# Kernel optimization log

Measured on AMD Instinct MI355X. Metric: run time of the kernel, lower is better.

## Reference

```python
import jax, jax.numpy as jnp
import numpy as np

N_NODES = 50000
EPS = 1e-5


def sage_conv_max(x, src, dst, W_l, b_l, W_r):
    # PyG SAGEConv(aggr='max'): out = lin_l(max_j x_j) + lin_r(x_i)
    msg = x[src]                                   # [E, d] gather
    agg = jnp.full((x.shape[0], x.shape[1]), -jnp.inf, dtype=x.dtype)
    agg = agg.at[dst].max(msg)                     # scatter-max over edges
    agg = jnp.where(jnp.isneginf(agg), 0.0, agg)   # isolated nodes -> 0 (PyG convention)
    return agg @ W_l.T + b_l + x @ W_r.T


def batch_norm(x, gamma, beta):
    mean = jnp.mean(x, axis=0)
    var = jnp.var(x, axis=0)
    return (x - mean) * jax.lax.rsqrt(var + EPS) * gamma + beta


def setup_inputs() -> dict:
    key = jax.random.key(0)
    ks = jax.random.split(key, 10)
    d_in, d_h, d_out = 128, 128, 32
    s = lambda fan: 1.0 / np.sqrt(fan)
    return {
        "x": jax.random.normal(ks[0], (N_NODES, d_in), dtype=jnp.float32),
        "edge_index": jax.random.randint(ks[1], (2, 800000), 0, N_NODES, dtype=jnp.int32),
        "W_l1": jax.random.uniform(ks[2], (d_h, d_in), jnp.float32, -s(d_in), s(d_in)),
        "b_l1": jnp.zeros((d_h,), jnp.float32),
        "W_r1": jax.random.uniform(ks[3], (d_h, d_in), jnp.float32, -s(d_in), s(d_in)),
        "gamma1": jnp.ones((d_h,), jnp.float32),
        "beta1": jnp.zeros((d_h,), jnp.float32),
        "W_l2": jax.random.uniform(ks[4], (d_out, d_h), jnp.float32, -s(d_h), s(d_h)),
        "b_l2": jnp.zeros((d_out,), jnp.float32),
        "W_r2": jax.random.uniform(ks[5], (d_out, d_h), jnp.float32, -s(d_h), s(d_h)),
    }


def reference(x, edge_index, W_l1, b_l1, W_r1, gamma1, beta1, W_l2, b_l2, W_r2):
    src, dst = edge_index[0], edge_index[1]
    h = sage_conv_max(x, src, dst, W_l1, b_l1, W_r1)
    h = batch_norm(h, gamma1, beta1)
    h = jax.nn.relu(h)
    # dropout is identity at inference
    return sage_conv_max(h, src, dst, W_l2, b_l2, W_r2)
```

## Files before the change

### kernel.cpp

```cpp
#include <hip/hip_runtime.h>
#include <math.h>
#include <float.h>

#define N_NODES 50000
#define N_EDGES 800000
#define DH 128
#define NB 196
#define EB 4096
#define NBUCK 98
#define BSH 9
#define CAP 80
#define SEGC 9216
#define CELLS_PER_BUCKET (NB * CAP)

typedef __attribute__((ext_vector_type(8))) short bf16x8;
typedef __attribute__((ext_vector_type(4))) float f32x4;

static __device__ __forceinline__ unsigned short f2bf(float f) {
  unsigned int u = __float_as_uint(f);
  u = (u + 0x7fff + ((u >> 16) & 1)) >> 16;
  return (unsigned short)u;
}

__global__ __launch_bounds__(256) void setup_kernel(
    const int* __restrict__ src, const int* __restrict__ dst,
    unsigned int* __restrict__ pairs,
    const float* __restrict__ x, const float* __restrict__ Wl1,
    const float* __restrict__ Wr1, const float* __restrict__ Wl2,
    const float* __restrict__ Wr2, unsigned int* __restrict__ x_bf,
    unsigned short* __restrict__ Wcat1, unsigned short* __restrict__ Wcat2,
    float* __restrict__ gsums) {
  const int b = blockIdx.x, tid = threadIdx.x;
  if (b < NB) {
    __shared__ int cur[NBUCK];
    if (tid < NBUCK) cur[tid] = 0;
    __syncthreads();
#pragma unroll
    for (int it = 0; it < EB / 256; ++it) {
      int e = b * EB + it * 256 + tid;
      if (e < N_EDGES) {
        int d = dst[e];
        int bk = d >> BSH;
        int p = atomicAdd(&cur[bk], 1);
        if (p < CAP)
          pairs[(size_t)(bk * NB + b) * CAP + p] =
              (unsigned)src[e] | ((unsigned)(d & 511) << 16);
      }
    }
    __syncthreads();
    for (int s = tid; s < NBUCK * CAP; s += 256) {
      int bk = s / CAP, slot = s - bk * CAP;
      if (slot >= cur[bk])
        pairs[(size_t)(bk * NB + b) * CAP + slot] = 0x80000000u;
    }
  } else if (b < NB + 6250) {
    int i = (b - NB) * 256 + tid;
    float4 v = ((const float4*)x)[i];
    uint2 o;
    o.x = (unsigned int)f2bf(v.x) | ((unsigned int)f2bf(v.y) << 16);
    o.y = (unsigned int)f2bf(v.z) | ((unsigned int)f2bf(v.w) << 16);
    ((uint2*)x_bf)[i] = o;
  } else if (b < NB + 6410) {
    int i = (b - NB - 6250) * 256 + tid;
    if (i < 32768) {
      int n = i >> 8, k = i & 255;
      float w = (k < 128) ? Wl1[n * 128 + k] : Wr1[n * 128 + (k - 128)];
      Wcat1[i] = f2bf(w);
    } else if (i < 40960) {
      int j = i - 32768;
      int n = j >> 8, k = j & 255;
      float w = (k < 128) ? Wl2[n * 128 + k] : Wr2[n * 128 + (k - 128)];
      Wcat2[j] = f2bf(w);
    }
  } else {
#pragma unroll
    for (int i = 0; i < 8; ++i) gsums[i * 256 + tid] = 0.f;
  }
}

__global__ __launch_bounds__(1024) void bucket_sort(const unsigned int* __restrict__ pairs,
                                                    unsigned int* __restrict__ rowinfo,
                                                    int* __restrict__ elist) {
  __shared__ int hist[512], sc[512], cpos[512];
  const int b = blockIdx.x, tid = threadIdx.x;
  const size_t s0 = (size_t)b * CELLS_PER_BUCKET;
  if (tid < 512) hist[tid] = 0;
  __syncthreads();
  for (int p = tid; p < CELLS_PER_BUCKET; p += 1024) {
    unsigned int pr = pairs[s0 + p];
    if ((int)pr >= 0) atomicAdd(&hist[(pr >> 16) & 511], 1);
  }
  __syncthreads();
  if (tid < 512) sc[tid] = hist[tid];
  __syncthreads();
  for (int off = 1; off < 512; off <<= 1) {
    int x = (tid < 512 && tid >= off) ? sc[tid - off] : 0;
    __syncthreads();
    if (tid < 512) sc[tid] += x;
    __syncthreads();
  }
  if (tid < 512) {
    int excl = sc[tid] - hist[tid];
    cpos[tid] = excl;
    int node = (b << BSH) + tid;
    if (node < N_NODES)
      rowinfo[node] = (unsigned)(b * SEGC + excl) | ((unsigned)hist[tid] << 20);
  }
  __syncthreads();
  for (int p = tid; p < CELLS_PER_BUCKET; p += 1024) {
    unsigned int pr = pairs[s0 + p];
    if ((int)pr >= 0) {
      int loc = atomicAdd(&cpos[(pr >> 16) & 511], 1);
      elist[b * SEGC + loc] = (int)(pr & 0xffffu);
    }
  }
}

template <bool BN>
__global__ __launch_bounds__(256) void agg_max_bf16(const uint4* __restrict__ feat4,
                                                    const unsigned int* __restrict__ rowinfo,
                                                    const int* __restrict__ elist,
                                                    const float* __restrict__ gsums,
                                                    const float* __restrict__ gamma,
                                                    const float* __restrict__ beta,
                                                    uint4* __restrict__ out4) {
  __shared__ float s_scale[128], s_shift[128];
  if (BN) {
    int t = threadIdx.x;
    if (t < 128) {
      float sm = 0.f, sq = 0.f;
#pragma unroll
      for (int r = 0; r < 8; ++r) {
        sm += gsums[r * 256 + t];
        sq += gsums[r * 256 + 128 + t];
      }
      const float inv = 1.f / (float)N_NODES;
      float mean = sm * inv;
      float var = sq * inv - mean * mean;
      float sc = gamma[t] * rsqrtf(var + 1e-5f);
      s_scale[t] = sc;
      s_shift[t] = beta[t] - mean * sc;
    }
    __syncthreads();
  }

  int node = blockIdx.x * 4 + (threadIdx.x >> 6);
  int lane = threadIdx.x & 63;
  int eslot = lane >> 4;
  int fq = lane & 15;
  unsigned int info = rowinfo[node];
  int e0 = (int)(info & 0xFFFFFu);
  int deg = (int)(info >> 20);
  int e1 = e0 + deg;
  float m[8];
#pragma unroll
  for (int j = 0; j < 8; ++j) m[j] = -FLT_MAX;

  if (deg > 0) {
    const int last = e1 - 1;
    for (int base = e0; base < e1; base += 16) {
      int idx[4];
#pragma unroll
      for (int q = 0; q < 4; ++q) {
        int e = base + q * 4 + eslot;
        if (e > last) e = last;
        idx[q] = elist[e];
      }
      uint4 v[4];
#pragma unroll
      for (int q = 0; q < 4; ++q) v[q] = feat4[(size_t)idx[q] * 16 + fq];
#pragma unroll
      for (int q = 0; q < 4; ++q) {
        const unsigned int* pv = (const unsigned int*)&v[q];
#pragma unroll
        for (int c = 0; c < 4; ++c) {
          m[2 * c]     = fmaxf(m[2 * c],     __uint_as_float(pv[c] << 16));
          m[2 * c + 1] = fmaxf(m[2 * c + 1], __uint_as_float(pv[c] & 0xffff0000u));
        }
      }
    }
  }

#pragma unroll
  for (int j = 0; j < 8; ++j) {
    m[j] = fmaxf(m[j], __shfl_xor(m[j], 16, 64));
    m[j] = fmaxf(m[j], __shfl_xor(m[j], 32, 64));
  }
  if (eslot == 0) {
    if (deg == 0) {
#pragma unroll
      for (int j = 0; j < 8; ++j) m[j] = 0.f;
    } else if (BN) {
#pragma unroll
      for (int j = 0; j < 8; ++j) {
        int col = fq * 8 + j;
        m[j] = fmaxf(m[j] * s_scale[col] + s_shift[col], 0.f);
      }
    }
    uint4 o;
    o.x = (unsigned)f2bf(m[0]) | ((unsigned)f2bf(m[1]) << 16);
    o.y = (unsigned)f2bf(m[2]) | ((unsigned)f2bf(m[3]) << 16);
    o.z = (unsigned)f2bf(m[4]) | ((unsigned)f2bf(m[5]) << 16);
    o.w = (unsigned)f2bf(m[6]) | ((unsigned)f2bf(m[7]) << 16);
    out4[(size_t)node * 16 + fq] = o;
  }
}

#define ASTR 264

template <int NT, bool BF16OUT, bool STATS, bool BNIN>
__global__ __launch_bounds__(256) void gemm_mfma(
    const unsigned short* __restrict__ Aa, const unsigned short* __restrict__ Ab,
    const unsigned short* __restrict__ Wcat, const float* __restrict__ bias,
    unsigned short* __restrict__ outb, float* __restrict__ outf,
    float* __restrict__ gsums, const float* __restrict__ gamma,
    const float* __restrict__ beta, int N) {
  __shared__ unsigned short Alds[128 * ASTR];
  __shared__ float s_sum[128], s_sq[128];
  __shared__ float s_scale[128], s_shift[128];
  const int tid = threadIdx.x;
  const int rowBase = blockIdx.x * 128;

  if (STATS && tid < 128) { s_sum[tid] = 0.f; s_sq[tid] = 0.f; }
  if (BNIN) {
    if (tid < 128) {
      float sm = 0.f, sq = 0.f;
#pragma unroll
      for (int r = 0; r < 8; ++r) {
        sm += gsums[r * 256 + tid];
        sq += gsums[r * 256 + 128 + tid];
      }
      const float inv = 1.f / (float)N_NODES;
      float mean = sm * inv;
      float var = sq * inv - mean * mean;
      float sc = gamma[tid] * rsqrtf(var + 1e-5f);
      s_scale[tid] = sc;
      s_shift[tid] = beta[tid] - mean * sc;
    }
    __syncthreads();
  }

#pragma unroll
  for (int it = 0; it < 16; ++it) {
    int f = tid + it * 256;
    int r = f >> 5;
    int seg = f & 31;
    int n = rowBase + r;
    if (n >= N) n = N - 1;
    const unsigned short* src = (seg < 16)
        ? (Aa + (size_t)n * 128 + seg * 8)
        : (Ab + (size_t)n * 128 + (seg - 16) * 8);
    int4 d = *(const int4*)src;
    if (BNIN && seg >= 16) {
      int kb = (seg - 16) * 8;
      unsigned int* dp = (unsigned int*)&d;
#pragma unroll
      for (int c = 0; c < 4; ++c) {
        int k0 = kb + 2 * c;
        float lo = __uint_as_float(dp[c] << 16);
        float hi = __uint_as_float(dp[c] & 0xffff0000u);
        lo = fmaxf(lo * s_scale[k0] + s_shift[k0], 0.f);
        hi = fmaxf(hi * s_scale[k0 + 1] + s_shift[k0 + 1], 0.f);
        dp[c] = (unsigned)f2bf(lo) | ((unsigned)f2bf(hi) << 16);
      }
    }
    *(int4*)(&Alds[r * ASTR + seg * 8]) = d;
  }
  __syncthreads();

  const int wv = tid >> 6;
  const int lane = tid & 63;
  const int ln15 = lane & 15;
  const int quad = lane >> 4;
  const int m0 = wv * 32;

  f32x4 acc[2][NT] = {};

#pragma unroll
  for (int ks = 0; ks < 8; ++ks) {
    const int k0 = ks * 32;
    bf16x8 a0 = *(const bf16x8*)(&Alds[(m0 + ln15) * ASTR + k0 + quad * 8]);
    bf16x8 a1 = *(const bf16x8*)(&Alds[(m0 + 16 + ln15) * ASTR + k0 + quad * 8]);
#pragma unroll
    for (int nt = 0; nt < NT; ++nt) {
      bf16x8 b = *(const bf16x8*)(Wcat + (size_t)(nt * 16 + ln15) * 256 + k0 + quad * 8);
      acc[0][nt] = __builtin_amdgcn_mfma_f32_16x16x32_bf16(a0, b, acc[0][nt], 0, 0, 0);
      acc[1][nt] = __builtin_amdgcn_mfma_f32_16x16x32_bf16(a1, b, acc[1][nt], 0, 0, 0);
    }
  }

  const int ldo = NT * 16;
#pragma unroll
  for (int nt = 0; nt < NT; ++nt) {
    int col = nt * 16 + ln15;
    float bv = bias[col];
    float psum = 0.f, psq = 0.f;
#pragma unroll
    for (int mt = 0; mt < 2; ++mt) {
#pragma unroll
      for (int i = 0; i < 4; ++i) {
        int r = rowBase + m0 + mt * 16 + quad * 4 + i;
        if (r < N) {
          float val = acc[mt][nt][i] + bv;
          if (STATS) { psum += val; psq += val * val; }
          if (BF16OUT)
            outb[(size_t)r * ldo + col] = f2bf(val);
          else
            outf[(size_t)r * ldo + col] = val;
        }
      }
    }
    if (STATS) {
      atomicAdd(&s_sum[col], psum);
      atomicAdd(&s_sq[col], psq);
    }
  }
  if (STATS) {
    __syncthreads();
    if (tid < 128) {
      int rep = blockIdx.x & 7;
      atomicAdd(&gsums[rep * 256 + tid], s_sum[tid]);
      atomicAdd(&gsums[rep * 256 + 128 + tid], s_sq[tid]);
    }
  }
}

extern "C" void kernel_launch(void* const* d_in, const int* in_sizes, int n_in,
                              void* d_out, int out_size, void* d_ws, size_t ws_size,
                              hipStream_t stream) {
  (void)in_sizes; (void)n_in; (void)out_size; (void)ws_size;
  const float* x     = (const float*)d_in[0];
  const int*   eidx  = (const int*)d_in[1];
  const float* W_l1  = (const float*)d_in[2];
  const float* b_l1  = (const float*)d_in[3];
  const float* W_r1  = (const float*)d_in[4];
  const float* gamma = (const float*)d_in[5];
  const float* beta  = (const float*)d_in[6];
  const float* W_l2  = (const float*)d_in[7];
  const float* b_l2  = (const float*)d_in[8];
  const float* W_r2  = (const float*)d_in[9];
  const int* srcp = eidx;
  const int* dstp = eidx + N_EDGES;
  float* out = (float*)d_out;

  int* wsi = (int*)d_ws;
  float* gsums   = (float*)wsi;
  unsigned int* rowinfo = (unsigned int*)(wsi + 2048);
  int*   elist   = wsi + 52064;
  unsigned int* pairs   = (unsigned int*)(wsi + 955232);
  unsigned int* x_bf    = (unsigned int*)(wsi + 2491872);
  unsigned int* agg_bf  = (unsigned int*)(wsi + 5691872);
  unsigned int* h_bf    = (unsigned int*)(wsi + 8891872);
  unsigned short* Wcat1 = (unsigned short*)(wsi + 12091872);
  unsigned short* Wcat2 = (unsigned short*)(wsi + 12108256);

  setup_kernel<<<dim3(NB + 6410 + 1), 256, 0, stream>>>(
      srcp, dstp, pairs, x, W_l1, W_r1, W_l2, W_r2, x_bf, Wcat1, Wcat2, gsums);

  bucket_sort<<<dim3(NBUCK), 1024, 0, stream>>>(pairs, rowinfo, elist);

  agg_max_bf16<false><<<dim3(N_NODES / 4), 256, 0, stream>>>(
      (const uint4*)x_bf, rowinfo, elist, nullptr, nullptr, nullptr, (uint4*)agg_bf);
  gemm_mfma<8, true, true, false><<<dim3(391), 256, 0, stream>>>(
      (const unsigned short*)agg_bf, (const unsigned short*)x_bf, Wcat1, b_l1,
      (unsigned short*)h_bf, nullptr, gsums, nullptr, nullptr, N_NODES);

  agg_max_bf16<true><<<dim3(N_NODES / 4), 256, 0, stream>>>(
      (const uint4*)h_bf, rowinfo, elist, gsums, gamma, beta, (uint4*)agg_bf);
  gemm_mfma<2, false, false, true><<<dim3(391), 256, 0, stream>>>(
      (const unsigned short*)agg_bf, (const unsigned short*)h_bf, Wcat2, b_l2,
      nullptr, out, gsums, gamma, beta, N_NODES);
}
```

Before: 222.4 us.

## Prefetch next edge batch in max aggregation; use wave-shuffle scan in bucket sort

The edge loop in the max-aggregation kernel now software-pipelines its gathers. It issues the feature loads for the next batch of 16 edges, plus the index loads for the batch after that, before reducing the current batch. This hides gather latency behind the max arithmetic, at the cost of extra registers for the second set of vectors. Separately, the 512-element prefix scan in bucket_sort is replaced by a warp-shuffle scan plus a small cross-wave scan. That removes about 18 block-wide barriers.

```diff
diff --git a/kernel.cpp b/kernel.cpp
--- a/kernel.cpp
+++ b/kernel.cpp
@@ -81,7 +81,8 @@
 __global__ __launch_bounds__(1024) void bucket_sort(const unsigned int* __restrict__ pairs,
                                                     unsigned int* __restrict__ rowinfo,
                                                     int* __restrict__ elist) {
-  __shared__ int hist[512], sc[512], cpos[512];
+  __shared__ int hist[512], cpos[512];
+  __shared__ int wsum[8];
   const int b = blockIdx.x, tid = threadIdx.x;
   const size_t s0 = (size_t)b * CELLS_PER_BUCKET;
   if (tid < 512) hist[tid] = 0;
@@ -91,20 +92,37 @@
     if ((int)pr >= 0) atomicAdd(&hist[(pr >> 16) & 511], 1);
   }
   __syncthreads();
-  if (tid < 512) sc[tid] = hist[tid];
-  __syncthreads();
-  for (int off = 1; off < 512; off <<= 1) {
-    int x = (tid < 512 && tid >= off) ? sc[tid - off] : 0;
-    __syncthreads();
-    if (tid < 512) sc[tid] += x;
-    __syncthreads();
-  }
+  int incl = 0, h = 0;
   if (tid < 512) {
-    int excl = sc[tid] - hist[tid];
+    const int l = tid & 63;
+    h = hist[tid];
+    incl = h;
+#pragma unroll
+    for (int off = 1; off < 64; off <<= 1) {
+      int t = __shfl_up(incl, off, 64);
+      if (l >= off) incl += t;
+    }
+    if (l == 63) wsum[tid >> 6] = incl;
+  }
+  __syncthreads();
+  if (tid < 64) {
+    int v = (tid < 8) ? wsum[tid] : 0;
+#pragma unroll
+    for (int off = 1; off < 8; off <<= 1) {
+      int t = __shfl_up(v, off, 64);
+      if (tid >= off) v += t;
+    }
+    if (tid < 8) wsum[tid] = v;
+  }
+  __syncthreads();
+  if (tid < 512) {
+    const int w = tid >> 6;
+    int tot = incl + ((w > 0) ? wsum[w - 1] : 0);
+    int excl = tot - h;
     cpos[tid] = excl;
     int node = (b << BSH) + tid;
     if (node < N_NODES)
-      rowinfo[node] = (unsigned)(b * SEGC + excl) | ((unsigned)hist[tid] << 20);
+      rowinfo[node] = (unsigned)(b * SEGC + excl) | ((unsigned)h << 20);
   }
   __syncthreads();
   for (int p = tid; p < CELLS_PER_BUCKET; p += 1024) {
@@ -158,25 +176,53 @@
 
   if (deg > 0) {
     const int last = e1 - 1;
-    for (int base = e0; base < e1; base += 16) {
-      int idx[4];
+    int idxN[4];
+#pragma unroll
+    for (int q = 0; q < 4; ++q) {
+      int e = e0 + q * 4 + eslot;
+      if (e > last) e = last;
+      idxN[q] = elist[e];
+    }
+    uint4 vC[4];
+#pragma unroll
+    for (int q = 0; q < 4; ++q)
+      vC[q] = feat4[(size_t)idxN[q] * 16 + fq];
+#pragma unroll
+    for (int q = 0; q < 4; ++q) {
+      int e = e0 + 16 + q * 4 + eslot;
+      if (e > last) e = last;
+      idxN[q] = elist[e];
+    }
+    for (int base = e0 + 16; base < e1; base += 16) {
+      uint4 vN[4];
+#pragma unroll
+      for (int q = 0; q < 4; ++q)
+        vN[q] = feat4[(size_t)idxN[q] * 16 + fq];
 #pragma unroll
       for (int q = 0; q < 4; ++q) {
-        int e = base + q * 4 + eslot;
+        int e = base + 16 + q * 4 + eslot;
         if (e > last) e = last;
-        idx[q] = elist[e];
-      }
-      uint4 v[4];
-#pragma unroll
-      for (int q = 0; q < 4; ++q) v[q] = feat4[(size_t)idx[q] * 16 + fq];
+        idxN[q] = elist[e];
+      }
 #pragma unroll
       for (int q = 0; q < 4; ++q) {
-        const unsigned int* pv = (const unsigned int*)&v[q];
+        const unsigned int* pv = (const unsigned int*)&vC[q];
 #pragma unroll
         for (int c = 0; c < 4; ++c) {
           m[2 * c]     = fmaxf(m[2 * c],     __uint_as_float(pv[c] << 16));
           m[2 * c + 1] = fmaxf(m[2 * c + 1], __uint_as_float(pv[c] & 0xffff0000u));
         }
+      }
+#pragma unroll
+      for (int q = 0; q < 4; ++q) vC[q] = vN[q];
+    }
+#pragma unroll
+    for (int q = 0; q < 4; ++q) {
+      const unsigned int* pv = (const unsigned int*)&vC[q];
+#pragma unroll
+      for (int c = 0; c < 4; ++c) {
+        m[2 * c]     = fmaxf(m[2 * c],     __uint_as_float(pv[c] << 16));
+        m[2 * c + 1] = fmaxf(m[2 * c + 1], __uint_as_float(pv[c] & 0xffff0000u));
       }
     }
   }
```

New measurement: 223.0 us. No clear change (+0.3%).

## Fuse max-aggregation into MFMA GEMM and use wave-shuffle scan in bucket sort

Applied to the files above, without the earlier changes.

The separate aggregation kernel is merged into the GEMM kernel. Each 64-row block gathers neighbour features, applies the max (and BN+ReLU for layer 2), and writes the aggregated row straight into LDS next to the self features, so the agg_bf buffer round-trip and two launches go away. The gather mapping changes from four edge slots per node with a cross-lane reduce to one 16-lane group per node walking edges serially. That gives fewer parallel loads in flight per node, and the tiles are half the size with more blocks. The bucket-sort prefix scan is also rewritten from an LDS Hillis-Steele scan with many barriers to a wave-shuffle scan.

```diff
diff --git a/kernel.cpp b/kernel.cpp
--- a/kernel.cpp
+++ b/kernel.cpp
@@ -12,6 +12,7 @@
 #define CAP 80
 #define SEGC 9216
 #define CELLS_PER_BUCKET (NB * CAP)
+#define NBLK 782
 
 typedef __attribute__((ext_vector_type(8))) short bf16x8;
 typedef __attribute__((ext_vector_type(4))) float f32x4;
@@ -81,7 +82,8 @@
 __global__ __launch_bounds__(1024) void bucket_sort(const unsigned int* __restrict__ pairs,
                                                     unsigned int* __restrict__ rowinfo,
                                                     int* __restrict__ elist) {
-  __shared__ int hist[512], sc[512], cpos[512];
+  __shared__ int hist[512], cpos[512];
+  __shared__ int wsum[8];
   const int b = blockIdx.x, tid = threadIdx.x;
   const size_t s0 = (size_t)b * CELLS_PER_BUCKET;
   if (tid < 512) hist[tid] = 0;
@@ -91,20 +93,37 @@
     if ((int)pr >= 0) atomicAdd(&hist[(pr >> 16) & 511], 1);
   }
   __syncthreads();
-  if (tid < 512) sc[tid] = hist[tid];
-  __syncthreads();
-  for (int off = 1; off < 512; off <<= 1) {
-    int x = (tid < 512 && tid >= off) ? sc[tid - off] : 0;
-    __syncthreads();
-    if (tid < 512) sc[tid] += x;
-    __syncthreads();
-  }
+  int incl = 0, h = 0;
   if (tid < 512) {
-    int excl = sc[tid] - hist[tid];
+    const int l = tid & 63;
+    h = hist[tid];
+    incl = h;
+#pragma unroll
+    for (int off = 1; off < 64; off <<= 1) {
+      int t = __shfl_up(incl, off, 64);
+      if (l >= off) incl += t;
+    }
+    if (l == 63) wsum[tid >> 6] = incl;
+  }
+  __syncthreads();
+  if (tid < 64) {
+    int v = (tid < 8) ? wsum[tid] : 0;
+#pragma unroll
+    for (int off = 1; off < 8; off <<= 1) {
+      int t = __shfl_up(v, off, 64);
+      if (tid >= off) v += t;
+    }
+    if (tid < 8) wsum[tid] = v;
+  }
+  __syncthreads();
+  if (tid < 512) {
+    const int w = tid >> 6;
+    int tot = incl + ((w > 0) ? wsum[w - 1] : 0);
+    int excl = tot - h;
     cpos[tid] = excl;
     int node = (b << BSH) + tid;
     if (node < N_NODES)
-      rowinfo[node] = (unsigned)(b * SEGC + excl) | ((unsigned)hist[tid] << 20);
+      rowinfo[node] = (unsigned)(b * SEGC + excl) | ((unsigned)h << 20);
   }
   __syncthreads();
   for (int p = tid; p < CELLS_PER_BUCKET; p += 1024) {
@@ -116,113 +135,26 @@
   }
 }
 
-template <bool BN>
-__global__ __launch_bounds__(256) void agg_max_bf16(const uint4* __restrict__ feat4,
-                                                    const unsigned int* __restrict__ rowinfo,
-                                                    const int* __restrict__ elist,
-                                                    const float* __restrict__ gsums,
-                                                    const float* __restrict__ gamma,
-                                                    const float* __restrict__ beta,
-                                                    uint4* __restrict__ out4) {
-  __shared__ float s_scale[128], s_shift[128];
-  if (BN) {
-    int t = threadIdx.x;
-    if (t < 128) {
-      float sm = 0.f, sq = 0.f;
-#pragma unroll
-      for (int r = 0; r < 8; ++r) {
-        sm += gsums[r * 256 + t];
-        sq += gsums[r * 256 + 128 + t];
-      }
-      const float inv = 1.f / (float)N_NODES;
-      float mean = sm * inv;
-      float var = sq * inv - mean * mean;
-      float sc = gamma[t] * rsqrtf(var + 1e-5f);
-      s_scale[t] = sc;
-      s_shift[t] = beta[t] - mean * sc;
-    }
-    __syncthreads();
-  }
-
-  int node = blockIdx.x * 4 + (threadIdx.x >> 6);
-  int lane = threadIdx.x & 63;
-  int eslot = lane >> 4;
-  int fq = lane & 15;
-  unsigned int info = rowinfo[node];
-  int e0 = (int)(info & 0xFFFFFu);
-  int deg = (int)(info >> 20);
-  int e1 = e0 + deg;
-  float m[8];
-#pragma unroll
-  for (int j = 0; j < 8; ++j) m[j] = -FLT_MAX;
-
-  if (deg > 0) {
-    const int last = e1 - 1;
-    for (int base = e0; base < e1; base += 16) {
-      int idx[4];
-#pragma unroll
-      for (int q = 0; q < 4; ++q) {
-        int e = base + q * 4 + eslot;
-        if (e > last) e = last;
-        idx[q] = elist[e];
-      }
-      uint4 v[4];
-#pragma unroll
-      for (int q = 0; q < 4; ++q) v[q] = feat4[(size_t)idx[q] * 16 + fq];
-#pragma unroll
-      for (int q = 0; q < 4; ++q) {
-        const unsigned int* pv = (const unsigned int*)&v[q];
-#pragma unroll
-        for (int c = 0; c < 4; ++c) {
-          m[2 * c]     = fmaxf(m[2 * c],     __uint_as_float(pv[c] << 16));
-          m[2 * c + 1] = fmaxf(m[2 * c + 1], __uint_as_float(pv[c] & 0xffff0000u));
-        }
-      }
-    }
-  }
-
-#pragma unroll
-  for (int j = 0; j < 8; ++j) {
-    m[j] = fmaxf(m[j], __shfl_xor(m[j], 16, 64));
-    m[j] = fmaxf(m[j], __shfl_xor(m[j], 32, 64));
-  }
-  if (eslot == 0) {
-    if (deg == 0) {
-#pragma unroll
-      for (int j = 0; j < 8; ++j) m[j] = 0.f;
-    } else if (BN) {
-#pragma unroll
-      for (int j = 0; j < 8; ++j) {
-        int col = fq * 8 + j;
-        m[j] = fmaxf(m[j] * s_scale[col] + s_shift[col], 0.f);
-      }
-    }
-    uint4 o;
-    o.x = (unsigned)f2bf(m[0]) | ((unsigned)f2bf(m[1]) << 16);
-    o.y = (unsigned)f2bf(m[2]) | ((unsigned)f2bf(m[3]) << 16);
-    o.z = (unsigned)f2bf(m[4]) | ((unsigned)f2bf(m[5]) << 16);
-    o.w = (unsigned)f2bf(m[6]) | ((unsigned)f2bf(m[7]) << 16);
-    out4[(size_t)node * 16 + fq] = o;
-  }
-}
-
 #define ASTR 264
 
-template <int NT, bool BF16OUT, bool STATS, bool BNIN>
-__global__ __launch_bounds__(256) void gemm_mfma(
-    const unsigned short* __restrict__ Aa, const unsigned short* __restrict__ Ab,
+template <int NT, bool BF16OUT, bool STATS, bool BN>
+__global__ __launch_bounds__(256) void fused_layer(
+    const uint4* __restrict__ feat4,
+    const unsigned short* __restrict__ Ab,
+    const unsigned int* __restrict__ rowinfo,
+    const int* __restrict__ elist,
     const unsigned short* __restrict__ Wcat, const float* __restrict__ bias,
     unsigned short* __restrict__ outb, float* __restrict__ outf,
     float* __restrict__ gsums, const float* __restrict__ gamma,
     const float* __restrict__ beta, int N) {
-  __shared__ unsigned short Alds[128 * ASTR];
+  __shared__ unsigned short Alds[64 * ASTR];
   __shared__ float s_sum[128], s_sq[128];
   __shared__ float s_scale[128], s_shift[128];
   const int tid = threadIdx.x;
-  const int rowBase = blockIdx.x * 128;
+  const int rowBase = blockIdx.x * 64;
 
   if (STATS && tid < 128) { s_sum[tid] = 0.f; s_sq[tid] = 0.f; }
-  if (BNIN) {
+  if (BN) {
     if (tid < 128) {
       float sm = 0.f, sq = 0.f;
 #pragma unroll
@@ -241,18 +173,14 @@
   }
 
 #pragma unroll
-  for (int it = 0; it < 16; ++it) {
+  for (int it = 0; it < 4; ++it) {
     int f = tid + it * 256;
-    int r = f >> 5;
-    int seg = f & 31;
+    int r = f >> 4, seg = f & 15;
     int n = rowBase + r;
     if (n >= N) n = N - 1;
-    const unsigned short* src = (seg < 16)
-        ? (Aa + (size_t)n * 128 + seg * 8)
-        : (Ab + (size_t)n * 128 + (seg - 16) * 8);
-    int4 d = *(const int4*)src;
-    if (BNIN && seg >= 16) {
-      int kb = (seg - 16) * 8;
+    int4 d = *(const int4*)(Ab + (size_t)n * 128 + seg * 8);
+    if (BN) {
+      int kb = seg * 8;
       unsigned int* dp = (unsigned int*)&d;
 #pragma unroll
       for (int c = 0; c < 4; ++c) {
@@ -264,28 +192,80 @@
         dp[c] = (unsigned)f2bf(lo) | ((unsigned)f2bf(hi) << 16);
       }
     }
-    *(int4*)(&Alds[r * ASTR + seg * 8]) = d;
-  }
-  __syncthreads();
+    *(int4*)(&Alds[r * ASTR + 128 + seg * 8]) = d;
+  }
 
   const int wv = tid >> 6;
+  const int g = (tid >> 4) & 3;
+  const int fq = tid & 15;
+#pragma unroll
+  for (int it = 0; it < 4; ++it) {
+    int r = it * 16 + wv * 4 + g;
+    int node = rowBase + r;
+    if (node >= N) node = N - 1;
+    unsigned int info = rowinfo[node];
+    int e0 = (int)(info & 0xFFFFFu);
+    int deg = (int)(info >> 20);
+    int e1 = e0 + deg;
+    const int last = e1 - 1;
+    float m[8];
+#pragma unroll
+    for (int j = 0; j < 8; ++j) m[j] = -FLT_MAX;
+    for (int base = e0; base < e1; base += 4) {
+      int idx[4];
+#pragma unroll
+      for (int q = 0; q < 4; ++q) {
+        int e = base + q;
+        if (e > last) e = last;
+        idx[q] = elist[e];
+      }
+      uint4 v[4];
+#pragma unroll
+      for (int q = 0; q < 4; ++q) v[q] = feat4[(size_t)idx[q] * 16 + fq];
+#pragma unroll
+      for (int q = 0; q < 4; ++q) {
+        const unsigned int* pv = (const unsigned int*)&v[q];
+#pragma unroll
+        for (int c = 0; c < 4; ++c) {
+          m[2 * c]     = fmaxf(m[2 * c],     __uint_as_float(pv[c] << 16));
+          m[2 * c + 1] = fmaxf(m[2 * c + 1], __uint_as_float(pv[c] & 0xffff0000u));
+        }
+      }
+    }
+    if (deg == 0) {
+#pragma unroll
+      for (int j = 0; j < 8; ++j) m[j] = 0.f;
+    } else if (BN) {
+#pragma unroll
+      for (int j = 0; j < 8; ++j) {
+        int col = fq * 8 + j;
+        m[j] = fmaxf(m[j] * s_scale[col] + s_shift[col], 0.f);
+      }
+    }
+    int4 o;
+    unsigned int* op = (unsigned int*)&o;
+    op[0] = (unsigned)f2bf(m[0]) | ((unsigned)f2bf(m[1]) << 16);
+    op[1] = (unsigned)f2bf(m[2]) | ((unsigned)f2bf(m[3]) << 16);
+    op[2] = (unsigned)f2bf(m[4]) | ((unsigned)f2bf(m[5]) << 16);
+    op[3] = (unsigned)f2bf(m[6]) | ((unsigned)f2bf(m[7]) << 16);
+    *(int4*)(&Alds[r * ASTR + fq * 8]) = o;
+  }
+  __syncthreads();
+
   const int lane = tid & 63;
   const int ln15 = lane & 15;
   const int quad = lane >> 4;
-  const int m0 = wv * 32;
-
-  f32x4 acc[2][NT] = {};
-
+  const int m0 = wv * 16;
+
+  f32x4 acc[NT] = {};
 #pragma unroll
   for (int ks = 0; ks < 8; ++ks) {
     const int k0 = ks * 32;
-    bf16x8 a0 = *(const bf16x8*)(&Alds[(m0 + ln15) * ASTR + k0 + quad * 8]);
-    bf16x8 a1 = *(const bf16x8*)(&Alds[(m0 + 16 + ln15) * ASTR + k0 + quad * 8]);
+    bf16x8 a = *(const bf16x8*)(&Alds[(m0 + ln15) * ASTR + k0 + quad * 8]);
 #pragma unroll
     for (int nt = 0; nt < NT; ++nt) {
       bf16x8 b = *(const bf16x8*)(Wcat + (size_t)(nt * 16 + ln15) * 256 + k0 + quad * 8);
-      acc[0][nt] = __builtin_amdgcn_mfma_f32_16x16x32_bf16(a0, b, acc[0][nt], 0, 0, 0);
-      acc[1][nt] = __builtin_amdgcn_mfma_f32_16x16x32_bf16(a1, b, acc[1][nt], 0, 0, 0);
+      acc[nt] = __builtin_amdgcn_mfma_f32_16x16x32_bf16(a, b, acc[nt], 0, 0, 0);
     }
   }
 
@@ -296,18 +276,15 @@
     float bv = bias[col];
     float psum = 0.f, psq = 0.f;
 #pragma unroll
-    for (int mt = 0; mt < 2; ++mt) {
-#pragma unroll
-      for (int i = 0; i < 4; ++i) {
-        int r = rowBase + m0 + mt * 16 + quad * 4 + i;
-        if (r < N) {
-          float val = acc[mt][nt][i] + bv;
-          if (STATS) { psum += val; psq += val * val; }
-          if (BF16OUT)
-            outb[(size_t)r * ldo + col] = f2bf(val);
-          else
-            outf[(size_t)r * ldo + col] = val;
-        }
+    for (int i = 0; i < 4; ++i) {
+      int r = rowBase + m0 + quad * 4 + i;
+      if (r < N) {
+        float val = acc[nt][i] + bv;
+        if (STATS) { psum += val; psq += val * val; }
+        if (BF16OUT)
+          outb[(size_t)r * ldo + col] = f2bf(val);
+        else
+          outf[(size_t)r * ldo + col] = val;
       }
     }
     if (STATS) {
@@ -349,7 +326,6 @@
   int*   elist   = wsi + 52064;
   unsigned int* pairs   = (unsigned int*)(wsi + 955232);
   unsigned int* x_bf    = (unsigned int*)(wsi + 2491872);
-  unsigned int* agg_bf  = (unsigned int*)(wsi + 5691872);
   unsigned int* h_bf    = (unsigned int*)(wsi + 8891872);
   unsigned short* Wcat1 = (unsigned short*)(wsi + 12091872);
   unsigned short* Wcat2 = (unsigned short*)(wsi + 12108256);
@@ -359,15 +335,11 @@
 
   bucket_sort<<<dim3(NBUCK), 1024, 0, stream>>>(pairs, rowinfo, elist);
 
-  agg_max_bf16<false><<<dim3(N_NODES / 4), 256, 0, stream>>>(
-      (const uint4*)x_bf, rowinfo, elist, nullptr, nullptr, nullptr, (uint4*)agg_bf);
-  gemm_mfma<8, true, true, false><<<dim3(391), 256, 0, stream>>>(
-      (const unsigned short*)agg_bf, (const unsigned short*)x_bf, Wcat1, b_l1,
+  fused_layer<8, true, true, false><<<dim3(NBLK), 256, 0, stream>>>(
+      (const uint4*)x_bf, (const unsigned short*)x_bf, rowinfo, elist, Wcat1, b_l1,
       (unsigned short*)h_bf, nullptr, gsums, nullptr, nullptr, N_NODES);
 
-  agg_max_bf16<true><<<dim3(N_NODES / 4), 256, 0, stream>>>(
-      (const uint4*)h_bf, rowinfo, elist, gsums, gamma, beta, (uint4*)agg_bf);
-  gemm_mfma<2, false, false, true><<<dim3(391), 256, 0, stream>>>(
-      (const unsigned short*)agg_bf, (const unsigned short*)h_bf, Wcat2, b_l2,
+  fused_layer<2, false, false, true><<<dim3(NBLK), 256, 0, stream>>>(
+      (const uint4*)h_bf, (const unsigned short*)h_bf, rowinfo, elist, Wcat2, b_l2,
       nullptr, out, gsums, gamma, beta, N_NODES);
 }
```

Measured after the change: 225.2 us. Within noise of the previous version (+1.3%).

## Split max-aggregation into feature slices with per-edge lanes; stage pair buckets in LDS

Applied to the files above, without the earlier changes.

The max-aggregation kernel now gives each block one 32-feature slice of 64 nodes. Sixteen lanes cover the slice and each 16-lane group walks one node's edges, four edges per step. Neighbouring block IDs share a slice, which is meant to improve L2 locality of the gathered feature columns, at the cost of narrower 4-byte loads instead of 16-byte loads. The setup kernel stages bucket pairs in LDS and writes each full cell once, replacing scattered global writes plus a separate padding pass. bucket_sort replaces its 512-element barrier-heavy scan with a wave-shuffle scan.

```diff
diff --git a/kernel.cpp b/kernel.cpp
--- a/kernel.cpp
+++ b/kernel.cpp
@@ -4,7 +4,6 @@
 
 #define N_NODES 50000
 #define N_EDGES 800000
-#define DH 128
 #define NB 196
 #define EB 4096
 #define NBUCK 98
@@ -12,6 +11,8 @@
 #define CAP 80
 #define SEGC 9216
 #define CELLS_PER_BUCKET (NB * CAP)
+#define GCHUNKS 784
+#define GGRID (GCHUNKS * 4)
 
 typedef __attribute__((ext_vector_type(8))) short bf16x8;
 typedef __attribute__((ext_vector_type(4))) float f32x4;
@@ -32,7 +33,9 @@
     float* __restrict__ gsums) {
   const int b = blockIdx.x, tid = threadIdx.x;
   if (b < NB) {
+    __shared__ unsigned int lp[NBUCK * CAP];
     __shared__ int cur[NBUCK];
+    for (int s = tid; s < NBUCK * CAP; s += 256) lp[s] = 0x80000000u;
     if (tid < NBUCK) cur[tid] = 0;
     __syncthreads();
 #pragma unroll
@@ -43,15 +46,13 @@
         int bk = d >> BSH;
         int p = atomicAdd(&cur[bk], 1);
         if (p < CAP)
-          pairs[(size_t)(bk * NB + b) * CAP + p] =
-              (unsigned)src[e] | ((unsigned)(d & 511) << 16);
+          lp[bk * CAP + p] = (unsigned)src[e] | ((unsigned)(d & 511) << 16);
       }
     }
     __syncthreads();
     for (int s = tid; s < NBUCK * CAP; s += 256) {
-      int bk = s / CAP, slot = s - bk * CAP;
-      if (slot >= cur[bk])
-        pairs[(size_t)(bk * NB + b) * CAP + slot] = 0x80000000u;
+      int bk = s / CAP, p = s - bk * CAP;
+      pairs[(size_t)(bk * NB + b) * CAP + p] = lp[s];
     }
   } else if (b < NB + 6250) {
     int i = (b - NB) * 256 + tid;
@@ -81,7 +82,8 @@
 __global__ __launch_bounds__(1024) void bucket_sort(const unsigned int* __restrict__ pairs,
                                                     unsigned int* __restrict__ rowinfo,
                                                     int* __restrict__ elist) {
-  __shared__ int hist[512], sc[512], cpos[512];
+  __shared__ int hist[512], cpos[512];
+  __shared__ int wsum[8];
   const int b = blockIdx.x, tid = threadIdx.x;
   const size_t s0 = (size_t)b * CELLS_PER_BUCKET;
   if (tid < 512) hist[tid] = 0;
@@ -91,20 +93,37 @@
     if ((int)pr >= 0) atomicAdd(&hist[(pr >> 16) & 511], 1);
   }
   __syncthreads();
-  if (tid < 512) sc[tid] = hist[tid];
-  __syncthreads();
-  for (int off = 1; off < 512; off <<= 1) {
-    int x = (tid < 512 && tid >= off) ? sc[tid - off] : 0;
-    __syncthreads();
-    if (tid < 512) sc[tid] += x;
-    __syncthreads();
-  }
+  int incl = 0, h = 0;
   if (tid < 512) {
-    int excl = sc[tid] - hist[tid];
+    const int l = tid & 63;
+    h = hist[tid];
+    incl = h;
+#pragma unroll
+    for (int off = 1; off < 64; off <<= 1) {
+      int t = __shfl_up(incl, off, 64);
+      if (l >= off) incl += t;
+    }
+    if (l == 63) wsum[tid >> 6] = incl;
+  }
+  __syncthreads();
+  if (tid < 64) {
+    int v = (tid < 8) ? wsum[tid] : 0;
+#pragma unroll
+    for (int off = 1; off < 8; off <<= 1) {
+      int t = __shfl_up(v, off, 64);
+      if (tid >= off) v += t;
+    }
+    if (tid < 8) wsum[tid] = v;
+  }
+  __syncthreads();
+  if (tid < 512) {
+    const int w = tid >> 6;
+    int tot = incl + ((w > 0) ? wsum[w - 1] : 0);
+    int excl = tot - h;
     cpos[tid] = excl;
     int node = (b << BSH) + tid;
     if (node < N_NODES)
-      rowinfo[node] = (unsigned)(b * SEGC + excl) | ((unsigned)hist[tid] << 20);
+      rowinfo[node] = (unsigned)(b * SEGC + excl) | ((unsigned)h << 20);
   }
   __syncthreads();
   for (int p = tid; p < CELLS_PER_BUCKET; p += 1024) {
@@ -117,92 +136,77 @@
 }
 
 template <bool BN>
-__global__ __launch_bounds__(256) void agg_max_bf16(const uint4* __restrict__ feat4,
-                                                    const unsigned int* __restrict__ rowinfo,
-                                                    const int* __restrict__ elist,
-                                                    const float* __restrict__ gsums,
-                                                    const float* __restrict__ gamma,
-                                                    const float* __restrict__ beta,
-                                                    uint4* __restrict__ out4) {
-  __shared__ float s_scale[128], s_shift[128];
+__global__ __launch_bounds__(256) void gather_slice(
+    const unsigned int* __restrict__ feat,
+    const unsigned int* __restrict__ rowinfo,
+    const int* __restrict__ elist,
+    const float* __restrict__ gsums,
+    const float* __restrict__ gamma, const float* __restrict__ beta,
+    unsigned int* __restrict__ out) {
+  __shared__ float s_scale[32], s_shift[32];
+  const int bid = blockIdx.x;
+  const int grp = bid & 7;
+  const int slice = grp >> 1;
+  const int chunk = ((bid >> 3) << 1) + (grp & 1);
+  const int tid = threadIdx.x;
   if (BN) {
-    int t = threadIdx.x;
-    if (t < 128) {
+    if (tid < 32) {
+      int f = slice * 32 + tid;
       float sm = 0.f, sq = 0.f;
 #pragma unroll
       for (int r = 0; r < 8; ++r) {
-        sm += gsums[r * 256 + t];
-        sq += gsums[r * 256 + 128 + t];
+        sm += gsums[r * 256 + f];
+        sq += gsums[r * 256 + 128 + f];
       }
       const float inv = 1.f / (float)N_NODES;
       float mean = sm * inv;
       float var = sq * inv - mean * mean;
-      float sc = gamma[t] * rsqrtf(var + 1e-5f);
-      s_scale[t] = sc;
-      s_shift[t] = beta[t] - mean * sc;
-    }
-    __syncthreads();
-  }
-
-  int node = blockIdx.x * 4 + (threadIdx.x >> 6);
-  int lane = threadIdx.x & 63;
-  int eslot = lane >> 4;
-  int fq = lane & 15;
-  unsigned int info = rowinfo[node];
-  int e0 = (int)(info & 0xFFFFFu);
-  int deg = (int)(info >> 20);
-  int e1 = e0 + deg;
-  float m[8];
-#pragma unroll
-  for (int j = 0; j < 8; ++j) m[j] = -FLT_MAX;
-
-  if (deg > 0) {
-    const int last = e1 - 1;
-    for (int base = e0; base < e1; base += 16) {
-      int idx[4];
-#pragma unroll
-      for (int q = 0; q < 4; ++q) {
-        int e = base + q * 4 + eslot;
-        if (e > last) e = last;
-        idx[q] = elist[e];
-      }
-      uint4 v[4];
-#pragma unroll
-      for (int q = 0; q < 4; ++q) v[q] = feat4[(size_t)idx[q] * 16 + fq];
-#pragma unroll
-      for (int q = 0; q < 4; ++q) {
-        const unsigned int* pv = (const unsigned int*)&v[q];
-#pragma unroll
-        for (int c = 0; c < 4; ++c) {
-          m[2 * c]     = fmaxf(m[2 * c],     __uint_as_float(pv[c] << 16));
-          m[2 * c + 1] = fmaxf(m[2 * c + 1], __uint_as_float(pv[c] & 0xffff0000u));
+      float sc = gamma[f] * rsqrtf(var + 1e-5f);
+      s_scale[tid] = sc;
+      s_shift[tid] = beta[f] - mean * sc;
+    }
+    __syncthreads();
+  }
+  const int g = tid >> 4;
+  const int fq = tid & 15;
+  const unsigned int* fs = feat + slice * 16 + fq;
+#pragma unroll
+  for (int it = 0; it < 4; ++it) {
+    int node = chunk * 64 + it * 16 + g;
+    if (node >= N_NODES) node = N_NODES - 1;
+    unsigned int info = rowinfo[node];
+    int e0 = (int)(info & 0xFFFFFu);
+    int deg = (int)(info >> 20);
+    float m0, m1;
+    if (deg > 0) {
+      m0 = -FLT_MAX; m1 = -FLT_MAX;
+      const int last = e0 + deg - 1;
+      for (int base = e0; base <= last; base += 4) {
+        int idx[4];
+#pragma unroll
+        for (int q = 0; q < 4; ++q) {
+          int e = base + q;
+          if (e > last) e = last;
+          idx[q] = elist[e];
         }
-      }
-    }
-  }
-
-#pragma unroll
-  for (int j = 0; j < 8; ++j) {
-    m[j] = fmaxf(m[j], __shfl_xor(m[j], 16, 64));
-    m[j] = fmaxf(m[j], __shfl_xor(m[j], 32, 64));
-  }
-  if (eslot == 0) {
-    if (deg == 0) {
-#pragma unroll
-      for (int j = 0; j < 8; ++j) m[j] = 0.f;
-    } else if (BN) {
-#pragma unroll
-      for (int j = 0; j < 8; ++j) {
-        int col = fq * 8 + j;
-        m[j] = fmaxf(m[j] * s_scale[col] + s_shift[col], 0.f);
-      }
-    }
-    uint4 o;
-    o.x = (unsigned)f2bf(m[0]) | ((unsigned)f2bf(m[1]) << 16);
-    o.y = (unsigned)f2bf(m[2]) | ((unsigned)f2bf(m[3]) << 16);
-    o.z = (unsigned)f2bf(m[4]) | ((unsigned)f2bf(m[5]) << 16);
-    o.w = (unsigned)f2bf(m[6]) | ((unsigned)f2bf(m[7]) << 16);
-    out4[(size_t)node * 16 + fq] = o;
+        unsigned int v[4];
+#pragma unroll
+        for (int q = 0; q < 4; ++q) v[q] = fs[(size_t)idx[q] * 64];
+#pragma unroll
+        for (int q = 0; q < 4; ++q) {
+          m0 = fmaxf(m0, __uint_as_float(v[q] << 16));
+          m1 = fmaxf(m1, __uint_as_float(v[q] & 0xffff0000u));
+        }
+      }
+      if (BN) {
+        m0 = fmaxf(m0 * s_scale[2 * fq] + s_shift[2 * fq], 0.f);
+        m1 = fmaxf(m1 * s_scale[2 * fq + 1] + s_shift[2 * fq + 1], 0.f);
+      }
+    } else {
+      m0 = 0.f; m1 = 0.f;
+    }
+    out[(size_t)node * 64 + slice * 16 + fq] =
+        (unsigned)f2bf(m0) | ((unsigned)f2bf(m1) << 16);
   }
 }
 
@@ -359,14 +363,16 @@
 
   bucket_sort<<<dim3(NBUCK), 1024, 0, stream>>>(pairs, rowinfo, elist);
 
-  agg_max_bf16<false><<<dim3(N_NODES / 4), 256, 0, stream>>>(
-      (const uint4*)x_bf, rowinfo, elist, nullptr, nullptr, nullptr, (uint4*)agg_bf);
+  gather_slice<false><<<dim3(GGRID), 256, 0, stream>>>(
+      x_bf, rowinfo, elist, nullptr, nullptr, nullptr, agg_bf);
+
   gemm_mfma<8, true, true, false><<<dim3(391), 256, 0, stream>>>(
       (const unsigned short*)agg_bf, (const unsigned short*)x_bf, Wcat1, b_l1,
       (unsigned short*)h_bf, nullptr, gsums, nullptr, nullptr, N_NODES);
 
-  agg_max_bf16<true><<<dim3(N_NODES / 4), 256, 0, stream>>>(
-      (const uint4*)h_bf, rowinfo, elist, gsums, gamma, beta, (uint4*)agg_bf);
+  gather_slice<true><<<dim3(GGRID), 256, 0, stream>>>(
+      h_bf, rowinfo, elist, gsums, gamma, beta, agg_bf);
+
   gemm_mfma<2, false, false, true><<<dim3(391), 256, 0, stream>>>(
       (const unsigned short*)agg_bf, (const unsigned short*)h_bf, Wcat2, b_l2,
       nullptr, out, gsums, gamma, beta, N_NODES);
```

Measured after the change: 246.5 us. +10.9%, slower.
